# Kernel tuning notes

Measured on AMD Instinct MI355X. Metric: run time of the kernel, lower is better.

The kernel has to match this reference:

```python
import jax, jax.numpy as jnp
import numpy as np

B, M, A, F = 8, 512, 16, 128  # batch, atoms/messages, irrep dim (n_ang_mom**2=16), feature channels
CG_DENSITY = 0.25             # CG coefficient tensors are highly sparse; emulate with a random mask


def setup_inputs() -> dict:
    key = jax.random.key(0)
    kx, ky, kc, km = jax.random.split(key, 4)
    x = jax.random.normal(kx, (B, M, A, F), dtype=jnp.float32)
    y = jax.random.normal(ky, (B, M, A, F), dtype=jnp.float32)
    # stand-in for cgc_multiplier(n_ang_mom): sparse [a, d, c] Clebsch-Gordan coefficient tensor
    cgc_dense = jax.random.normal(kc, (A, A, A), dtype=jnp.float32)
    mask = jax.random.bernoulli(km, CG_DENSITY, (A, A, A))
    cgc = jnp.where(mask, cgc_dense, 0.0)
    return {"x": x, "y": y, "cgc": cgc}


def reference(x, y, cgc):
    # TensorProductContractionLayer.call: triple contraction over irrep indices a, c
    # x: [b,m,a,f], y: [b,m,c,f], cgc: [a,d,c] -> res: [b,m,d,f]
    return jnp.einsum('bmaf,bmcf,adc->bmdf', x, y, cgc)
```

## Files before the change

kernel.cpp:

```cpp
#include <hip/hip_runtime.h>
#include <hip/hip_bf16.h>


typedef __attribute__((ext_vector_type(8))) short  short8;
typedef __attribute__((ext_vector_type(4))) float  floatx4;
typedef __attribute__((ext_vector_type(4))) unsigned int uintx4;

#define AA 16
#define FF 128
#define BM_PER_BLOCK 4

static __device__ __forceinline__ unsigned int pack_bf16_2(float lo, float hi) {
    __hip_bfloat162 h = __float22bfloat162_rn(make_float2(lo, hi));
    unsigned int u;
    __builtin_memcpy(&u, &h, 4);
    return u;
}

static __device__ __forceinline__ void gload_lds16(const float* g, float* l) {
    __builtin_amdgcn_global_load_lds(
        (const __attribute__((address_space(1))) void*)g,
        (__attribute__((address_space(3))) void*)l,
        16, 0, 0);
}

__global__ __launch_bounds__(256, 4)
void tpc_mfma_pipe_kernel(const float* __restrict__ x,
                          const float* __restrict__ y,
                          const float* __restrict__ cgc,
                          float* __restrict__ out) {
    __shared__ float lx[2][AA * FF];
    __shared__ float ly[2][AA * FF];

    const int tid  = threadIdx.x;
    const int w    = tid >> 6;
    const int lane = tid & 63;
    const int L    = lane & 15;
    const int quad = lane >> 4;
    const int qh   = quad >> 1;
    const int c0   = (quad & 1) * 8;

    const int bm0 = blockIdx.x * BM_PER_BLOCK;
    const size_t stride = (size_t)(AA * FF);
    const int off = w * 512 + lane * 4;

    {
        const float* xb = x + (size_t)bm0 * stride;
        const float* yb = y + (size_t)bm0 * stride;
        gload_lds16(xb + off,       &lx[0][off]);
        gload_lds16(xb + off + 256, &lx[0][off + 256]);
        gload_lds16(yb + off,       &ly[0][off]);
        gload_lds16(yb + off + 256, &ly[0][off + 256]);
    }

    short8 wfrag[8];
#pragma unroll
    for (int t = 0; t < 8; ++t) {
        const float* wp = cgc + (2 * t + qh) * (AA * AA) + L * AA + c0;
        const floatx4 w0 = *(const floatx4*)(wp);
        const floatx4 w1 = *(const floatx4*)(wp + 4);
        uintx4 u;
        u.x = pack_bf16_2(w0.x, w0.y);
        u.y = pack_bf16_2(w0.z, w0.w);
        u.z = pack_bf16_2(w1.x, w1.y);
        u.w = pack_bf16_2(w1.z, w1.w);
        wfrag[t] = __builtin_bit_cast(short8, u);
    }

    __syncthreads();

    const int f0 = w * 32 + L;

#pragma unroll
    for (int i = 0; i < BM_PER_BLOCK; ++i) {
        const int cur = i & 1;

        if (i + 1 < BM_PER_BLOCK) {
            const int nxt = (i + 1) & 1;
            const float* xb = x + (size_t)(bm0 + i + 1) * stride;
            const float* yb = y + (size_t)(bm0 + i + 1) * stride;
            gload_lds16(xb + off,       &lx[nxt][off]);
            gload_lds16(xb + off + 256, &lx[nxt][off + 256]);
            gload_lds16(yb + off,       &ly[nxt][off]);
            gload_lds16(yb + off + 256, &ly[nxt][off + 256]);
        }

        const float* lxc = lx[cur];
        const float* lyc = ly[cur];

        float xvA[8], xvB[8], yvA[8], yvB[8];
#pragma unroll
        for (int j = 0; j < 8; ++j) {
            yvA[j] = lyc[(c0 + j) * FF + f0];
            yvB[j] = lyc[(c0 + j) * FF + f0 + 16];
        }
#pragma unroll
        for (int t = 0; t < 8; ++t) {
            xvA[t] = lxc[(2 * t + qh) * FF + f0];
            xvB[t] = lxc[(2 * t + qh) * FF + f0 + 16];
        }

        floatx4 acc0 = {0.f, 0.f, 0.f, 0.f};
        floatx4 acc1 = {0.f, 0.f, 0.f, 0.f};
#pragma unroll
        for (int t = 0; t < 8; ++t) {
            uintx4 u;
            float xs = xvA[t];
            u.x = pack_bf16_2(xs * yvA[0], xs * yvA[1]);
            u.y = pack_bf16_2(xs * yvA[2], xs * yvA[3]);
            u.z = pack_bf16_2(xs * yvA[4], xs * yvA[5]);
            u.w = pack_bf16_2(xs * yvA[6], xs * yvA[7]);
            acc0 = __builtin_amdgcn_mfma_f32_16x16x32_bf16(
                       wfrag[t], __builtin_bit_cast(short8, u), acc0, 0, 0, 0);

            xs = xvB[t];
            u.x = pack_bf16_2(xs * yvB[0], xs * yvB[1]);
            u.y = pack_bf16_2(xs * yvB[2], xs * yvB[3]);
            u.z = pack_bf16_2(xs * yvB[4], xs * yvB[5]);
            u.w = pack_bf16_2(xs * yvB[6], xs * yvB[7]);
            acc1 = __builtin_amdgcn_mfma_f32_16x16x32_bf16(
                       wfrag[t], __builtin_bit_cast(short8, u), acc1, 0, 0, 0);
        }

        float* ob = out + (size_t)(bm0 + i) * stride;
#pragma unroll
        for (int r = 0; r < 4; ++r) {
            const int row = (quad * 4 + r) * FF;
            ob[row + f0]      = acc0[r];
            ob[row + f0 + 16] = acc1[r];
        }

        __syncthreads();
    }
}

extern "C" void kernel_launch(void* const* d_in, const int* in_sizes, int n_in,
                              void* d_out, int out_size, void* d_ws, size_t ws_size,
                              hipStream_t stream) {
    const float* x   = (const float*)d_in[0];
    const float* y   = (const float*)d_in[1];
    const float* cgc = (const float*)d_in[2];
    float* out = (float*)d_out;

    hipLaunchKernelGGL(tpc_mfma_pipe_kernel, dim3(1024), dim3(256), 0, stream,
                       x, y, cgc, out);
}
```

Measured before the change: 106.8 us.

## Drop LDS staging, assign one bm per wave with register prefetch and fp16 packed math

Replaces the LDS double-buffered pipeline with direct global loads into registers, mapping each wave to one (b,m) slice and iterating over four 32-wide feature chunks with software prefetch of the next chunk. Products are computed in packed fp16 after round-toward-zero conversion, and fp16 MFMA replaces the bf16 path, cutting float multiply and pack instructions. This removes block-wide barriers and LDS traffic, but the global loads are narrower (16 consecutive floats per row). The fp16 products also risk overflow or precision loss compared with products formed in fp32.

```diff
diff --git a/kernel.cpp b/kernel.cpp
--- a/kernel.cpp
+++ b/kernel.cpp
@@ -1,37 +1,24 @@
 #include <hip/hip_runtime.h>
-#include <hip/hip_bf16.h>
 
 
-typedef __attribute__((ext_vector_type(8))) short  short8;
-typedef __attribute__((ext_vector_type(4))) float  floatx4;
-typedef __attribute__((ext_vector_type(4))) unsigned int uintx4;
+typedef __attribute__((ext_vector_type(2))) _Float16 half2v;
+typedef __attribute__((ext_vector_type(8))) _Float16 half8;
+typedef __attribute__((ext_vector_type(4))) float    floatx4;
 
 #define AA 16
 #define FF 128
-#define BM_PER_BLOCK 4
 
-static __device__ __forceinline__ unsigned int pack_bf16_2(float lo, float hi) {
-    __hip_bfloat162 h = __float22bfloat162_rn(make_float2(lo, hi));
-    unsigned int u;
-    __builtin_memcpy(&u, &h, 4);
-    return u;
-}
+union H8 { half2v h2[4]; half8 h8; };
 
-static __device__ __forceinline__ void gload_lds16(const float* g, float* l) {
-    __builtin_amdgcn_global_load_lds(
-        (const __attribute__((address_space(1))) void*)g,
-        (__attribute__((address_space(3))) void*)l,
-        16, 0, 0);
+static __device__ __forceinline__ half2v pkrtz(float a, float b) {
+    return __builtin_bit_cast(half2v, __builtin_amdgcn_cvt_pkrtz(a, b));
 }
 
 __global__ __launch_bounds__(256, 4)
-void tpc_mfma_pipe_kernel(const float* __restrict__ x,
-                          const float* __restrict__ y,
-                          const float* __restrict__ cgc,
-                          float* __restrict__ out) {
-    __shared__ float lx[2][AA * FF];
-    __shared__ float ly[2][AA * FF];
-
+void tpc_mfma_direct_kernel(const float* __restrict__ x,
+                            const float* __restrict__ y,
+                            const float* __restrict__ cgc,
+                            float* __restrict__ out) {
     const int tid  = threadIdx.x;
     const int w    = tid >> 6;
     const int lane = tid & 63;
@@ -40,97 +27,92 @@
     const int qh   = quad >> 1;
     const int c0   = (quad & 1) * 8;
 
-    const int bm0 = blockIdx.x * BM_PER_BLOCK;
+    const int bm = blockIdx.x * 4 + w;
     const size_t stride = (size_t)(AA * FF);
-    const int off = w * 512 + lane * 4;
+    const float* xb = x + (size_t)bm * stride;
+    const float* yb = y + (size_t)bm * stride;
+    float*       ob = out + (size_t)bm * stride;
 
-    {
-        const float* xb = x + (size_t)bm0 * stride;
-        const float* yb = y + (size_t)bm0 * stride;
-        gload_lds16(xb + off,       &lx[0][off]);
-        gload_lds16(xb + off + 256, &lx[0][off + 256]);
-        gload_lds16(yb + off,       &ly[0][off]);
-        gload_lds16(yb + off + 256, &ly[0][off + 256]);
+    float xA[8], xB[8], yA[8], yB[8];
+#pragma unroll
+    for (int t = 0; t < 8; ++t) {
+        xA[t] = xb[(2 * t + qh) * FF + L];
+        xB[t] = xb[(2 * t + qh) * FF + L + 16];
+    }
+#pragma unroll
+    for (int j = 0; j < 8; ++j) {
+        yA[j] = yb[(c0 + j) * FF + L];
+        yB[j] = yb[(c0 + j) * FF + L + 16];
     }
 
-    short8 wfrag[8];
+    half8 wfrag[8];
 #pragma unroll
     for (int t = 0; t < 8; ++t) {
         const float* wp = cgc + (2 * t + qh) * (AA * AA) + L * AA + c0;
         const floatx4 w0 = *(const floatx4*)(wp);
         const floatx4 w1 = *(const floatx4*)(wp + 4);
-        uintx4 u;
-        u.x = pack_bf16_2(w0.x, w0.y);
-        u.y = pack_bf16_2(w0.z, w0.w);
-        u.z = pack_bf16_2(w1.x, w1.y);
-        u.w = pack_bf16_2(w1.z, w1.w);
-        wfrag[t] = __builtin_bit_cast(short8, u);
+        H8 wa;
+        wa.h2[0] = pkrtz(w0.x, w0.y);
+        wa.h2[1] = pkrtz(w0.z, w0.w);
+        wa.h2[2] = pkrtz(w1.x, w1.y);
+        wa.h2[3] = pkrtz(w1.z, w1.w);
+        wfrag[t] = wa.h8;
     }
 
-    __syncthreads();
-
-    const int f0 = w * 32 + L;
-
+    for (int g = 0; g < 4; ++g) {
+        half2v yp0[4], yp1[4];
 #pragma unroll
-    for (int i = 0; i < BM_PER_BLOCK; ++i) {
-        const int cur = i & 1;
-
-        if (i + 1 < BM_PER_BLOCK) {
-            const int nxt = (i + 1) & 1;
-            const float* xb = x + (size_t)(bm0 + i + 1) * stride;
-            const float* yb = y + (size_t)(bm0 + i + 1) * stride;
-            gload_lds16(xb + off,       &lx[nxt][off]);
-            gload_lds16(xb + off + 256, &lx[nxt][off + 256]);
-            gload_lds16(yb + off,       &ly[nxt][off]);
-            gload_lds16(yb + off + 256, &ly[nxt][off + 256]);
+        for (int jj = 0; jj < 4; ++jj) {
+            yp0[jj] = pkrtz(yA[2 * jj], yA[2 * jj + 1]);
+            yp1[jj] = pkrtz(yB[2 * jj], yB[2 * jj + 1]);
+        }
+        half2v xp0[8], xp1[8];
+#pragma unroll
+        for (int t = 0; t < 8; ++t) {
+            xp0[t] = pkrtz(xA[t], xA[t]);
+            xp1[t] = pkrtz(xB[t], xB[t]);
         }
 
-        const float* lxc = lx[cur];
-        const float* lyc = ly[cur];
-
-        float xvA[8], xvB[8], yvA[8], yvB[8];
+        if (g < 3) {
+            const int fA = (g + 1) * 32 + L;
 #pragma unroll
-        for (int j = 0; j < 8; ++j) {
-            yvA[j] = lyc[(c0 + j) * FF + f0];
-            yvB[j] = lyc[(c0 + j) * FF + f0 + 16];
-        }
+            for (int t = 0; t < 8; ++t) {
+                xA[t] = xb[(2 * t + qh) * FF + fA];
+                xB[t] = xb[(2 * t + qh) * FF + fA + 16];
+            }
 #pragma unroll
-        for (int t = 0; t < 8; ++t) {
-            xvA[t] = lxc[(2 * t + qh) * FF + f0];
-            xvB[t] = lxc[(2 * t + qh) * FF + f0 + 16];
+            for (int j = 0; j < 8; ++j) {
+                yA[j] = yb[(c0 + j) * FF + fA];
+                yB[j] = yb[(c0 + j) * FF + fA + 16];
+            }
         }
 
         floatx4 acc0 = {0.f, 0.f, 0.f, 0.f};
         floatx4 acc1 = {0.f, 0.f, 0.f, 0.f};
 #pragma unroll
         for (int t = 0; t < 8; ++t) {
-            uintx4 u;
-            float xs = xvA[t];
-            u.x = pack_bf16_2(xs * yvA[0], xs * yvA[1]);
-            u.y = pack_bf16_2(xs * yvA[2], xs * yvA[3]);
-            u.z = pack_bf16_2(xs * yvA[4], xs * yvA[5]);
-            u.w = pack_bf16_2(xs * yvA[6], xs * yvA[7]);
-            acc0 = __builtin_amdgcn_mfma_f32_16x16x32_bf16(
-                       wfrag[t], __builtin_bit_cast(short8, u), acc0, 0, 0, 0);
+            H8 b0;
+            b0.h2[0] = xp0[t] * yp0[0];
+            b0.h2[1] = xp0[t] * yp0[1];
+            b0.h2[2] = xp0[t] * yp0[2];
+            b0.h2[3] = xp0[t] * yp0[3];
+            acc0 = __builtin_amdgcn_mfma_f32_16x16x32_f16(wfrag[t], b0.h8, acc0, 0, 0, 0);
 
-            xs = xvB[t];
-            u.x = pack_bf16_2(xs * yvB[0], xs * yvB[1]);
-            u.y = pack_bf16_2(xs * yvB[2], xs * yvB[3]);
-            u.z = pack_bf16_2(xs * yvB[4], xs * yvB[5]);
-            u.w = pack_bf16_2(xs * yvB[6], xs * yvB[7]);
-            acc1 = __builtin_amdgcn_mfma_f32_16x16x32_bf16(
-                       wfrag[t], __builtin_bit_cast(short8, u), acc1, 0, 0, 0);
+            H8 b1;
+            b1.h2[0] = xp1[t] * yp1[0];
+            b1.h2[1] = xp1[t] * yp1[1];
+            b1.h2[2] = xp1[t] * yp1[2];
+            b1.h2[3] = xp1[t] * yp1[3];
+            acc1 = __builtin_amdgcn_mfma_f32_16x16x32_f16(wfrag[t], b1.h8, acc1, 0, 0, 0);
         }
 
-        float* ob = out + (size_t)(bm0 + i) * stride;
+        const int f0 = g * 32 + L;
 #pragma unroll
         for (int r = 0; r < 4; ++r) {
             const int row = (quad * 4 + r) * FF;
             ob[row + f0]      = acc0[r];
             ob[row + f0 + 16] = acc1[r];
         }
-
-        __syncthreads();
     }
 }
 
@@ -142,6 +124,6 @@
     const float* cgc = (const float*)d_in[2];
     float* out = (float*)d_out;
 
-    hipLaunchKernelGGL(tpc_mfma_pipe_kernel, dim3(1024), dim3(256), 0, stream,
+    hipLaunchKernelGGL(tpc_mfma_direct_kernel, dim3(1024), dim3(256), 0, stream,
                        x, y, cgc, out);
 }
```

Measured after the change: 108.3 us. Within noise of the previous version (+1.4%).
